# Performance work log

Measured on AMD Instinct MI355X. Metric: run time of the kernel, lower is better.

The kernel has to match this reference:

```python
import jax, jax.numpy as jnp
import numpy as np

N = 50000          # nodes
E = 1_600_000      # edges (avg degree 32)
IN = 16            # in_node_features
H0 = 64            # hidden_features_mlp[0]
D = 32             # hidden_features_mlp[1] == hidden_features_gnn
HF = 64            # hidden_final
OUT = 3            # out_features (congestion classes)
L = 3              # gnn_layer_num
EPS = 1e-5


def gelu(x):
    return jax.nn.gelu(x, approximate=False)  # torch nn.GELU default (erf)


def bn_eval(x, g, b):
    # BatchNorm1d in eval mode with fresh running stats (mean=0, var=1)
    return x * (g / jnp.sqrt(1.0 + EPS)) + b


def ln(x, g, b):
    m = jnp.mean(x, axis=-1, keepdims=True)
    v = jnp.var(x, axis=-1, keepdims=True)
    return (x - m) / jnp.sqrt(v + EPS) * g + b


def setup_inputs() -> dict:
    key = jax.random.key(0)
    ks = jax.random.split(key, 24)
    s = 0.1
    inp = {
        "x": jax.random.normal(ks[0], (N, IN), dtype=jnp.float32),
        "edge_index": jax.random.randint(ks[1], (2, E), 0, N, dtype=jnp.int32),
        # node_emb_mlp
        "emb_W1": jax.random.normal(ks[2], (IN, H0), dtype=jnp.float32) * s,
        "emb_b1": jnp.zeros((H0,), jnp.float32),
        "emb_bn1_g": jnp.ones((H0,), jnp.float32),
        "emb_bn1_b": jnp.zeros((H0,), jnp.float32),
        "emb_W2": jax.random.normal(ks[3], (H0, D), dtype=jnp.float32) * s,
        "emb_b2": jnp.zeros((D,), jnp.float32),
        "emb_bn2_g": jnp.ones((D,), jnp.float32),
        "emb_bn2_b": jnp.zeros((D,), jnp.float32),
        # GNN layers (stacked over L)
        "msg_W": jax.random.normal(ks[4], (L, 2 * D, D), dtype=jnp.float32) * s,
        "msg_b": jnp.zeros((L, D), jnp.float32),
        "msg_ln_g": jnp.ones((L, D), jnp.float32),
        "msg_ln_b": jnp.zeros((L, D), jnp.float32),
        "upd_W": jax.random.normal(ks[5], (L, 2 * D, D), dtype=jnp.float32) * s,
        "upd_b": jnp.zeros((L, D), jnp.float32),
        "upd_ln_g": jnp.ones((L, D), jnp.float32),
        "upd_ln_b": jnp.zeros((L, D), jnp.float32),
        # final_aggregation_layer
        "fin_W1": jax.random.normal(ks[6], (D, HF), dtype=jnp.float32) * s,
        "fin_b1": jnp.zeros((HF,), jnp.float32),
        "fin_bn_g": jnp.ones((HF,), jnp.float32),
        "fin_bn_b": jnp.zeros((HF,), jnp.float32),
        "fin_W2": jax.random.normal(ks[7], (HF, OUT), dtype=jnp.float32) * s,
        "fin_b2": jnp.zeros((OUT,), jnp.float32),
    }
    return inp


def reference(x, edge_index,
              emb_W1, emb_b1, emb_bn1_g, emb_bn1_b,
              emb_W2, emb_b2, emb_bn2_g, emb_bn2_b,
              msg_W, msg_b, msg_ln_g, msg_ln_b,
              upd_W, upd_b, upd_ln_g, upd_ln_b,
              fin_W1, fin_b1, fin_bn_g, fin_bn_b, fin_W2, fin_b2):
    src = edge_index[0]  # x_j (source, messages flow source->target)
    dst = edge_index[1]  # x_i (target, aggregation index)

    # node embedding MLP (dropout = identity in eval)
    h = gelu(bn_eval(x @ emb_W1 + emb_b1, emb_bn1_g, emb_bn1_b))
    h = gelu(bn_eval(h @ emb_W2 + emb_b2, emb_bn2_g, emb_bn2_b))
    pre = h

    for l in range(L):
        x_i = h[dst]  # [E, D]
        x_j = h[src]  # [E, D]
        m = gelu(ln(jnp.concatenate([x_i, x_j], axis=-1) @ msg_W[l] + msg_b[l],
                    msg_ln_g[l], msg_ln_b[l]))                 # [E, D]
        agg = jax.ops.segment_sum(m, dst, num_segments=N)      # [N, D]
        h = h + gelu(ln(jnp.concatenate([h, agg], axis=-1) @ upd_W[l] + upd_b[l],
                        upd_ln_g[l], upd_ln_b[l]))

    h = h + pre  # residual around the GNN stack

    general_emb = h[dst] - h[src]  # node_emb_j - node_emb_i, [E, D]
    out = gelu(bn_eval(general_emb @ fin_W1 + fin_b1, fin_bn_g, fin_bn_b))
    out = out @ fin_W2 + fin_b2  # [E, OUT] cc_scores
    return out
```

## Files before the change

### kernel.cpp

```cpp
#include <hip/hip_runtime.h>

#define NN 50000
#define NE 1600000
constexpr float LN_EPS = 1e-5f;

typedef _Float16 half8 __attribute__((ext_vector_type(8)));

__device__ __forceinline__ float gelu_f(float x){
  float ax = fabsf(x) * 0.70710678118654752440f;
  float t  = __builtin_amdgcn_rcpf(fmaf(0.3275911f, ax, 1.0f));
  float e  = __expf(-ax*ax);
  float p  = t*fmaf(t, fmaf(t, fmaf(t, fmaf(t, 1.061405429f, -1.453152027f),
                                    1.421413741f), -0.284496736f), 0.254829592f);
  float er = fmaf(-p, e, 1.0f);
  return 0.5f * x * (1.0f + copysignf(er, x));
}

__global__ __launch_bounds__(256) void hist_kernel(const int* __restrict__ ei,
    int* __restrict__ cnt, int* __restrict__ rank){
  int t = blockIdx.x*256 + threadIdx.x;
  if(t < NE/4){
    int4 d = ((const int4*)(ei + NE))[t];
    int4 r;
    r.x = atomicAdd(&cnt[d.x],1);
    r.y = atomicAdd(&cnt[d.y],1);
    r.z = atomicAdd(&cnt[d.z],1);
    r.w = atomicAdd(&cnt[d.w],1);
    ((int4*)rank)[t] = r;
  }
}

#define CHUNK 52
__global__ __launch_bounds__(1024) void scan_kernel(const int* __restrict__ deg, int* __restrict__ row_ptr){
  __shared__ int sums[1024];
  int t = threadIdx.x;
  int base = t*CHUNK;
  int4 v[13];
  int ssum = 0;
  #pragma unroll
  for(int i=0;i<13;i++){
    int idx = base + 4*i;
    if(idx + 3 < NN){
      v[i] = ((const int4*)deg)[(base>>2)+i];
    } else {
      v[i].x = (idx+0<NN)?deg[idx+0]:0; v[i].y = (idx+1<NN)?deg[idx+1]:0;
      v[i].z = (idx+2<NN)?deg[idx+2]:0; v[i].w = (idx+3<NN)?deg[idx+3]:0;
    }
    ssum += v[i].x + v[i].y + v[i].z + v[i].w;
  }
  sums[t]=ssum;
  __syncthreads();
  for(int off=1; off<1024; off<<=1){
    int vv = (t>=off) ? sums[t-off] : 0;
    __syncthreads();
    sums[t] += vv;
    __syncthreads();
  }
  int run = (t>0) ? sums[t-1] : 0;
  #pragma unroll
  for(int i=0;i<13;i++){
    int idx = base + 4*i;
    int4 o;
    o.x = run; run += v[i].x;
    o.y = run; run += v[i].y;
    o.z = run; run += v[i].z;
    o.w = run; run += v[i].w;
    if(idx + 3 < NN){
      ((int4*)row_ptr)[(base>>2)+i] = o;
    } else {
      if(idx+0<NN) row_ptr[idx+0]=o.x;
      if(idx+1<NN) row_ptr[idx+1]=o.y;
      if(idx+2<NN) row_ptr[idx+2]=o.z;
      if(idx+3<NN) row_ptr[idx+3]=o.w;
    }
  }
  if(t==1023) row_ptr[NN] = sums[1023];
}

__global__ __launch_bounds__(256) void fill_kernel(const int* __restrict__ ei,
    const int* __restrict__ row_ptr, const int* __restrict__ rank, int* __restrict__ csr_src){
  int t = blockIdx.x*256 + threadIdx.x;
  if(t < NE/4){
    int4 d  = ((const int4*)(ei + NE))[t];
    int4 sv = ((const int4*)ei)[t];
    int4 rk = ((const int4*)rank)[t];
    csr_src[row_ptr[d.x] + rk.x] = sv.x;
    csr_src[row_ptr[d.y] + rk.y] = sv.y;
    csr_src[row_ptr[d.z] + rk.z] = sv.z;
    csr_src[row_ptr[d.w] + rk.w] = sv.w;
  }
}

__global__ __launch_bounds__(256) void embed_pqr_kernel(
    const float* __restrict__ x,
    const float* __restrict__ W1, const float* __restrict__ b1,
    const float* __restrict__ g1, const float* __restrict__ bb1,
    const float* __restrict__ W2, const float* __restrict__ b2,
    const float* __restrict__ g2, const float* __restrict__ bb2,
    const float* __restrict__ Wm, const float* __restrict__ bm,
    const float* __restrict__ Wu, const float* __restrict__ bu,
    const float* __restrict__ fb1, const float* __restrict__ fbng, const float* __restrict__ fbnb,
    float* __restrict__ h, float* __restrict__ pre,
    float* __restrict__ P, _Float16* __restrict__ Qh, float* __restrict__ R,
    float* __restrict__ cvec)
{
  int n = blockIdx.x*256 + threadIdx.x;
  const float rs = rsqrtf(1.0f + LN_EPS);
  if(n < 64) cvec[n] = fmaf(fb1[n], fbng[n]*rs, fbnb[n]);
  if(n >= NN) return;
  float xv[16];
  const float4* xp = (const float4*)(x + (size_t)n*16);
  #pragma unroll
  for(int i=0;i<4;i++){ float4 t=xp[i]; xv[4*i]=t.x; xv[4*i+1]=t.y; xv[4*i+2]=t.z; xv[4*i+3]=t.w; }
  float a1[64];
  #pragma unroll
  for(int j=0;j<64;j++) a1[j]=b1[j];
  #pragma unroll
  for(int k=0;k<16;k++){
    float xk=xv[k];
    #pragma unroll
    for(int j=0;j<64;j++) a1[j] += xk * W1[k*64+j];
  }
  #pragma unroll
  for(int j=0;j<64;j++) a1[j] = gelu_f(a1[j]*(g1[j]*rs) + bb1[j]);
  float hv[32];
  #pragma unroll
  for(int j=0;j<32;j++) hv[j]=b2[j];
  #pragma unroll
  for(int k=0;k<64;k++){
    float tk=a1[k];
    #pragma unroll
    for(int j=0;j<32;j++) hv[j] += tk * W2[k*32+j];
  }
  #pragma unroll
  for(int j=0;j<32;j++){
    hv[j] = gelu_f(hv[j]*(g2[j]*rs) + bb2[j]);
    h[(size_t)n*32+j]=hv[j]; pre[(size_t)n*32+j]=hv[j];
  }
  float ap[32], aq[32], ar[32];
  #pragma unroll
  for(int j=0;j<32;j++){ ap[j]=bm[j]; aq[j]=0.f; ar[j]=bu[j]; }
  #pragma unroll
  for(int k=0;k<32;k++){
    float hk = hv[k];
    #pragma unroll
    for(int j=0;j<32;j++){
      ap[j] += hk * Wm[k*32+j];
      aq[j] += hk * Wm[(32+k)*32+j];
      ar[j] += hk * Wu[k*32+j];
    }
  }
  #pragma unroll
  for(int j=0;j<32;j++){ P[(size_t)n*32+j]=ap[j]; R[(size_t)n*32+j]=ar[j]; }
  half8* qo = (half8*)(Qh + (size_t)n*32);
  #pragma unroll
  for(int i=0;i<4;i++){
    half8 q;
    #pragma unroll
    for(int k=0;k<8;k++) q[k] = (_Float16)aq[8*i+k];
    qo[i] = q;
  }
}

__global__ __launch_bounds__(256) void msg_kernel(
    const float* __restrict__ P, const _Float16* __restrict__ Qh,
    const int* __restrict__ row_ptr, const int* __restrict__ csr_src,
    const float* __restrict__ mg, const float* __restrict__ mb,
    float* __restrict__ aggO)
{
  int tid = blockIdx.x*256 + threadIdx.x;
  int n = tid >> 4;
  int s = tid & 15;
  int slot = s >> 2;
  int q = s & 3;
  float4 mg0 = *(const float4*)(mg + q*8);
  float4 mg1 = *(const float4*)(mg + q*8 + 4);
  float4 mb0 = *(const float4*)(mb + q*8);
  float4 mb1 = *(const float4*)(mb + q*8 + 4);
  float mgq[8] = {mg0.x,mg0.y,mg0.z,mg0.w,mg1.x,mg1.y,mg1.z,mg1.w};
  float mbq[8] = {mb0.x,mb0.y,mb0.z,mb0.w,mb1.x,mb1.y,mb1.z,mb1.w};
  float4 pl0 = *(const float4*)(P + (size_t)n*32 + q*8);
  float4 pl1 = *(const float4*)(P + (size_t)n*32 + q*8 + 4);
  float p8[8] = {pl0.x,pl0.y,pl0.z,pl0.w,pl1.x,pl1.y,pl1.z,pl1.w};
  float agg8[8] = {0,0,0,0,0,0,0,0};
  int e0 = row_ptr[n], e1 = row_ptr[n+1];
  int e = e0 + slot;
  int src = (e < e1) ? csr_src[e] : 0;
  half8 qv = *(const half8*)(Qh + (size_t)src*32 + q*8);
  while(e < e1){
    int e2 = e + 4;
    int src2 = (e2 < e1) ? csr_src[e2] : 0;
    half8 qv2 = *(const half8*)(Qh + (size_t)src2*32 + q*8);
    float v[8];
    #pragma unroll
    for(int k=0;k<8;k++) v[k] = p8[k] + (float)qv[k];
    float ps = ((v[0]+v[1])+(v[2]+v[3])) + ((v[4]+v[5])+(v[6]+v[7]));
    ps += __shfl_xor(ps,1); ps += __shfl_xor(ps,2);
    float mean = ps * 0.03125f;
    float vs = 0.f;
    #pragma unroll
    for(int k=0;k<8;k++){ float dd = v[k]-mean; vs += dd*dd; v[k]=dd; }
    vs += __shfl_xor(vs,1); vs += __shfl_xor(vs,2);
    float rstd = rsqrtf(vs*0.03125f + LN_EPS);
    #pragma unroll
    for(int k=0;k<8;k++) agg8[k] += gelu_f(v[k]*rstd*mgq[k] + mbq[k]);
    qv = qv2; e = e2;
  }
  #pragma unroll
  for(int k=0;k<8;k++) agg8[k] += __shfl_xor(agg8[k], 4);
  #pragma unroll
  for(int k=0;k<8;k++) agg8[k] += __shfl_xor(agg8[k], 8);
  if(slot==0){
    float4 s0; s0.x=agg8[0]; s0.y=agg8[1]; s0.z=agg8[2]; s0.w=agg8[3];
    float4 s1; s1.x=agg8[4]; s1.y=agg8[5]; s1.z=agg8[6]; s1.w=agg8[7];
    *(float4*)(aggO + (size_t)n*32 + q*8)     = s0;
    *(float4*)(aggO + (size_t)n*32 + q*8 + 4) = s1;
  }
}

__global__ __launch_bounds__(256) void upd_pqr_kernel(
    const float* __restrict__ aggI, const float* __restrict__ Rio,
    const float* __restrict__ Ub,
    const float* __restrict__ ug, const float* __restrict__ ub,
    const float* __restrict__ Wm2, const float* __restrict__ bm2,
    const float* __restrict__ Wu2, const float* __restrict__ bu2,
    float* __restrict__ h,
    float* __restrict__ P, _Float16* __restrict__ Qh, float* __restrict__ Rout)
{
  int n = blockIdx.x*256 + threadIdx.x;
  if(n >= NN) return;
  float agg[32], u[32];
  const float4* ap4 = (const float4*)(aggI + (size_t)n*32);
  const float4* rp4 = (const float4*)(Rio + (size_t)n*32);
  #pragma unroll
  for(int i=0;i<8;i++){ float4 t=ap4[i]; agg[4*i]=t.x; agg[4*i+1]=t.y; agg[4*i+2]=t.z; agg[4*i+3]=t.w; }
  #pragma unroll
  for(int i=0;i<8;i++){ float4 t=rp4[i]; u[4*i]=t.x; u[4*i+1]=t.y; u[4*i+2]=t.z; u[4*i+3]=t.w; }
  #pragma unroll
  for(int k=0;k<32;k++){
    float a = agg[k];
    #pragma unroll
    for(int j=0;j<32;j++) u[j] += a * Ub[k*32+j];
  }
  float s0=0,s1=0,s2=0,s3=0;
  #pragma unroll
  for(int i=0;i<8;i++){ s0+=u[4*i]; s1+=u[4*i+1]; s2+=u[4*i+2]; s3+=u[4*i+3]; }
  float mean = ((s0+s1)+(s2+s3)) * 0.03125f;
  s0=s1=s2=s3=0.f;
  #pragma unroll
  for(int i=0;i<8;i++){
    float d0=u[4*i]-mean, d1=u[4*i+1]-mean, d2=u[4*i+2]-mean, d3=u[4*i+3]-mean;
    s0+=d0*d0; s1+=d1*d1; s2+=d2*d2; s3+=d3*d3;
    u[4*i]=d0; u[4*i+1]=d1; u[4*i+2]=d2; u[4*i+3]=d3;
  }
  float rstd = rsqrtf(((s0+s1)+(s2+s3))*0.03125f + LN_EPS);
  float hv[32];
  const float4* hp4 = (const float4*)(h + (size_t)n*32);
  #pragma unroll
  for(int i=0;i<8;i++){ float4 t=hp4[i]; hv[4*i]=t.x; hv[4*i+1]=t.y; hv[4*i+2]=t.z; hv[4*i+3]=t.w; }
  #pragma unroll
  for(int j=0;j<32;j++) hv[j] += gelu_f(u[j]*rstd*ug[j] + ub[j]);
  float4* ho = (float4*)(h + (size_t)n*32);
  #pragma unroll
  for(int i=0;i<8;i++){ float4 t; t.x=hv[4*i]; t.y=hv[4*i+1]; t.z=hv[4*i+2]; t.w=hv[4*i+3]; ho[i]=t; }
  float pq[32], qq[32], rr[32];
  #pragma unroll
  for(int j=0;j<32;j++){ pq[j]=bm2[j]; qq[j]=0.f; rr[j]=bu2[j]; }
  #pragma unroll
  for(int k=0;k<32;k++){
    float hk = hv[k];
    #pragma unroll
    for(int j=0;j<32;j++){
      pq[j] += hk * Wm2[k*32+j];
      qq[j] += hk * Wm2[(32+k)*32+j];
      rr[j] += hk * Wu2[k*32+j];
    }
  }
  #pragma unroll
  for(int j=0;j<32;j++){ P[(size_t)n*32+j]=pq[j]; Rout[(size_t)n*32+j]=rr[j]; }
  half8* qo = (half8*)(Qh + (size_t)n*32);
  #pragma unroll
  for(int i=0;i<4;i++){
    half8 q;
    #pragma unroll
    for(int k=0;k<8;k++) q[k] = (_Float16)qq[8*i+k];
    qo[i] = q;
  }
}

__global__ __launch_bounds__(256) void upd_fin_kernel(
    const float* __restrict__ aggI, const float* __restrict__ Rio,
    const float* __restrict__ Ub,
    const float* __restrict__ ug, const float* __restrict__ ub,
    const float* __restrict__ h, const float* __restrict__ pre,
    const float* __restrict__ fW1, const float* __restrict__ fbng,
    _Float16* __restrict__ y1, _Float16* __restrict__ y2)
{
  int n = blockIdx.x*256 + threadIdx.x;
  if(n >= NN) return;
  const float rs = rsqrtf(1.0f + LN_EPS);
  float agg[32], u[32];
  const float4* ap4 = (const float4*)(aggI + (size_t)n*32);
  const float4* rp4 = (const float4*)(Rio + (size_t)n*32);
  #pragma unroll
  for(int i=0;i<8;i++){ float4 t=ap4[i]; agg[4*i]=t.x; agg[4*i+1]=t.y; agg[4*i+2]=t.z; agg[4*i+3]=t.w; }
  #pragma unroll
  for(int i=0;i<8;i++){ float4 t=rp4[i]; u[4*i]=t.x; u[4*i+1]=t.y; u[4*i+2]=t.z; u[4*i+3]=t.w; }
  #pragma unroll
  for(int k=0;k<32;k++){
    float a = agg[k];
    #pragma unroll
    for(int j=0;j<32;j++) u[j] += a * Ub[k*32+j];
  }
  float s0=0,s1=0,s2=0,s3=0;
  #pragma unroll
  for(int i=0;i<8;i++){ s0+=u[4*i]; s1+=u[4*i+1]; s2+=u[4*i+2]; s3+=u[4*i+3]; }
  float mean = ((s0+s1)+(s2+s3)) * 0.03125f;
  s0=s1=s2=s3=0.f;
  #pragma unroll
  for(int i=0;i<8;i++){
    float d0=u[4*i]-mean, d1=u[4*i+1]-mean, d2=u[4*i+2]-mean, d3=u[4*i+3]-mean;
    s0+=d0*d0; s1+=d1*d1; s2+=d2*d2; s3+=d3*d3;
    u[4*i]=d0; u[4*i+1]=d1; u[4*i+2]=d2; u[4*i+3]=d3;
  }
  float rstd = rsqrtf(((s0+s1)+(s2+s3))*0.03125f + LN_EPS);
  float hv[32];
  const float4* hp4 = (const float4*)(h + (size_t)n*32);
  const float4* pp4 = (const float4*)(pre + (size_t)n*32);
  #pragma unroll
  for(int i=0;i<8;i++){ float4 t=hp4[i]; hv[4*i]=t.x; hv[4*i+1]=t.y; hv[4*i+2]=t.z; hv[4*i+3]=t.w; }
  #pragma unroll
  for(int j=0;j<32;j++) hv[j] += gelu_f(u[j]*rstd*ug[j] + ub[j]);
  #pragma unroll
  for(int i=0;i<8;i++){ float4 t=pp4[i]; hv[4*i]+=t.x; hv[4*i+1]+=t.y; hv[4*i+2]+=t.z; hv[4*i+3]+=t.w; }
  float acc[64];
  #pragma unroll
  for(int j=0;j<64;j++) acc[j]=0.f;
  #pragma unroll
  for(int k=0;k<32;k++){
    float hk = hv[k];
    #pragma unroll
    for(int j=0;j<64;j++) acc[j] += hk * fW1[k*64+j];
  }
  half8* yo1 = (half8*)(y1 + (size_t)n*32);
  half8* yo2 = (half8*)(y2 + (size_t)n*32);
  #pragma unroll
  for(int i=0;i<4;i++){
    half8 qa, qb;
    #pragma unroll
    for(int k=0;k<8;k++){
      qa[k] = (_Float16)(acc[8*i+k]    * (fbng[8*i+k]*rs));
      qb[k] = (_Float16)(acc[32+8*i+k] * (fbng[32+8*i+k]*rs));
    }
    yo1[i] = qa; yo2[i] = qb;
  }
}

__global__ __launch_bounds__(256) void finalA_kernel(
    const _Float16* __restrict__ y, const int* __restrict__ ei,
    const float* __restrict__ cvec, const float* __restrict__ W2,
    const float* __restrict__ b2, float* __restrict__ out)
{
  int t = blockIdx.x*256 + threadIdx.x;
  int e = t >> 2, q = t & 3;
  int s = __builtin_nontemporal_load(ei + e);
  int d = __builtin_nontemporal_load(ei + NE + e);
  half8 a8 = *(const half8*)(y + (size_t)d*32 + q*8);
  half8 c8 = *(const half8*)(y + (size_t)s*32 + q*8);
  float4 cv0 = *(const float4*)(cvec + q*8);
  float4 cv1 = *(const float4*)(cvec + q*8 + 4);
  float cq[8] = {cv0.x,cv0.y,cv0.z,cv0.w,cv1.x,cv1.y,cv1.z,cv1.w};
  const float4* wp = (const float4*)(W2 + q*24);
  float4 w0=wp[0], w1=wp[1], w2=wp[2], w3=wp[3], w4=wp[4], w5=wp[5];
  float w[24] = {w0.x,w0.y,w0.z,w0.w, w1.x,w1.y,w1.z,w1.w, w2.x,w2.y,w2.z,w2.w,
                 w3.x,w3.y,w3.z,w3.w, w4.x,w4.y,w4.z,w4.w, w5.x,w5.y,w5.z,w5.w};
  float o0=0.f,o1=0.f,o2=0.f;
  #pragma unroll
  for(int k=0;k<8;k++){
    float tt = gelu_f(((float)a8[k]-(float)c8[k]) + cq[k]);
    o0 += tt*w[3*k]; o1 += tt*w[3*k+1]; o2 += tt*w[3*k+2];
  }
  o0 += __shfl_xor(o0,1); o0 += __shfl_xor(o0,2);
  o1 += __shfl_xor(o1,1); o1 += __shfl_xor(o1,2);
  o2 += __shfl_xor(o2,1); o2 += __shfl_xor(o2,2);
  float ov = (q==0) ? o0 + b2[0] : (q==1) ? o1 + b2[1] : o2 + b2[2];
  if(q < 3) __builtin_nontemporal_store(ov, out + (size_t)e*3 + q);
}

__global__ __launch_bounds__(256) void finalB_kernel(
    const _Float16* __restrict__ y, const int* __restrict__ ei,
    const float* __restrict__ cvec,
    const float* __restrict__ W2,
    float* __restrict__ out)
{
  int t = blockIdx.x*256 + threadIdx.x;
  int e = t >> 2, q = t & 3;
  float prev = 0.f;
  if(q < 3) prev = __builtin_nontemporal_load(out + (size_t)e*3 + q);
  int s = __builtin_nontemporal_load(ei + e);
  int d = __builtin_nontemporal_load(ei + NE + e);
  half8 a8 = *(const half8*)(y + (size_t)d*32 + q*8);
  half8 c8 = *(const half8*)(y + (size_t)s*32 + q*8);
  float4 cv0 = *(const float4*)(cvec + q*8);
  float4 cv1 = *(const float4*)(cvec + q*8 + 4);
  float cq[8] = {cv0.x,cv0.y,cv0.z,cv0.w,cv1.x,cv1.y,cv1.z,cv1.w};
  const float4* wp = (const float4*)(W2 + q*24);
  float4 w0=wp[0], w1=wp[1], w2=wp[2], w3=wp[3], w4=wp[4], w5=wp[5];
  float w[24] = {w0.x,w0.y,w0.z,w0.w, w1.x,w1.y,w1.z,w1.w, w2.x,w2.y,w2.z,w2.w,
                 w3.x,w3.y,w3.z,w3.w, w4.x,w4.y,w4.z,w4.w, w5.x,w5.y,w5.z,w5.w};
  float o0=0.f,o1=0.f,o2=0.f;
  #pragma unroll
  for(int k=0;k<8;k++){
    float tt = gelu_f(((float)a8[k]-(float)c8[k]) + cq[k]);
    o0 += tt*w[3*k]; o1 += tt*w[3*k+1]; o2 += tt*w[3*k+2];
  }
  o0 += __shfl_xor(o0,1); o0 += __shfl_xor(o0,2);
  o1 += __shfl_xor(o1,1); o1 += __shfl_xor(o1,2);
  o2 += __shfl_xor(o2,1); o2 += __shfl_xor(o2,2);
  float ov = prev + ((q==0) ? o0 : (q==1) ? o1 : o2);
  if(q < 3) __builtin_nontemporal_store(ov, out + (size_t)e*3 + q);
}

extern "C" void kernel_launch(void* const* d_in, const int* in_sizes, int n_in,
                              void* d_out, int out_size, void* d_ws, size_t ws_size,
                              hipStream_t stream)
{
  (void)in_sizes; (void)n_in; (void)out_size; (void)ws_size;
  const float* x     = (const float*)d_in[0];
  const int*   ei    = (const int*)d_in[1];
  const float* eW1   = (const float*)d_in[2];
  const float* eb1   = (const float*)d_in[3];
  const float* ebn1g = (const float*)d_in[4];
  const float* ebn1b = (const float*)d_in[5];
  const float* eW2   = (const float*)d_in[6];
  const float* eb2   = (const float*)d_in[7];
  const float* ebn2g = (const float*)d_in[8];
  const float* ebn2b = (const float*)d_in[9];
  const float* msgW  = (const float*)d_in[10];
  const float* msgb  = (const float*)d_in[11];
  const float* msglng= (const float*)d_in[12];
  const float* msglnb= (const float*)d_in[13];
  const float* updW  = (const float*)d_in[14];
  const float* updb  = (const float*)d_in[15];
  const float* updlng= (const float*)d_in[16];
  const float* updlnb= (const float*)d_in[17];
  const float* fW1   = (const float*)d_in[18];
  const float* fb1   = (const float*)d_in[19];
  const float* fbng  = (const float*)d_in[20];
  const float* fbnb  = (const float*)d_in[21];
  const float* fW2   = (const float*)d_in[22];
  const float* fb2   = (const float*)d_in[23];
  float* out = (float*)d_out;

  float* f   = (float*)d_ws;
  float* h   = f;
  float* pre = f + 1*(size_t)NN*32;
  float* P   = f + 2*(size_t)NN*32;
  float* R   = f + 3*(size_t)NN*32;
  float* agg = f + 4*(size_t)NN*32;
  _Float16* Qh = (_Float16*)(f + 5*(size_t)NN*32);
  _Float16* y1 = (_Float16*)P;
  _Float16* y2 = y1 + (size_t)NN*32;
  int* ip      = (int*)(f + 5*(size_t)NN*32 + (size_t)NN*16);
  int* cnt     = ip;
  int* row_ptr = ip + NN;
  int* csr     = ip + 2*NN + 4;
  int* rank    = (int*)agg;
  float* cvec  = (float*)cnt;

  hipMemsetAsync(cnt, 0, NN*sizeof(int), stream);
  hist_kernel<<<(NE/4+255)/256, 256, 0, stream>>>(ei, cnt, rank);
  scan_kernel<<<1, 1024, 0, stream>>>(cnt, row_ptr);
  fill_kernel<<<(NE/4+255)/256, 256, 0, stream>>>(ei, row_ptr, rank, csr);

  embed_pqr_kernel<<<(NN+255)/256, 256, 0, stream>>>(x, eW1, eb1, ebn1g, ebn1b,
      eW2, eb2, ebn2g, ebn2b,
      msgW, msgb, updW, updb,
      fb1, fbng, fbnb,
      h, pre, P, Qh, R, cvec);

  for(int l=0; l<3; l++){
    msg_kernel<<<(NN*16)/256, 256, 0, stream>>>(P, Qh, row_ptr, csr,
        msglng + l*32, msglnb + l*32, agg);
    if(l < 2){
      upd_pqr_kernel<<<(NN+255)/256, 256, 0, stream>>>(agg, R,
          updW + l*2048 + 1024, updlng + l*32, updlnb + l*32,
          msgW + (l+1)*2048, msgb + (l+1)*32,
          updW + (l+1)*2048, updb + (l+1)*32,
          h, P, Qh, R);
    } else {
      upd_fin_kernel<<<(NN+255)/256, 256, 0, stream>>>(agg, R,
          updW + l*2048 + 1024, updlng + l*32, updlnb + l*32,
          h, pre, fW1, fbng, y1, y2);
    }
  }

  finalA_kernel<<<(NE*4)/256, 256, 0, stream>>>(y1, ei, cvec,      fW2,      fb2, out);
  finalB_kernel<<<(NE*4)/256, 256, 0, stream>>>(y2, ei, cvec + 32, fW2 + 96, out);
}
```

Before: 544.8 us.

## Split node MLPs across 4 lanes per node and fuse histogram with embedding

The per-node embedding, update and final-projection kernels now assign four lanes to each node, with lane shuffles broadcasting inputs, instead of one thread computing all 32–64 outputs. This cuts register pressure and raises occupancy and memory coalescing. The histogram pass and the embedding pass now run in a single launch by splitting the block range, which removes one launch and lets the two overlap. In exchange there is extra shuffle traffic, each lane re-reads the weight slices, and cvec moves to its own workspace slot so it no longer overlaps cnt.

```diff
diff --git a/kernel.cpp b/kernel.cpp
--- a/kernel.cpp
+++ b/kernel.cpp
@@ -2,6 +2,8 @@
 
 #define NN 50000
 #define NE 1600000
+#define HIST_B 1563
+#define EMB_B  782
 constexpr float LN_EPS = 1e-5f;
 
 typedef _Float16 half8 __attribute__((ext_vector_type(8)));
@@ -16,18 +18,109 @@
   return 0.5f * x * (1.0f + copysignf(er, x));
 }
 
-__global__ __launch_bounds__(256) void hist_kernel(const int* __restrict__ ei,
-    int* __restrict__ cnt, int* __restrict__ rank){
-  int t = blockIdx.x*256 + threadIdx.x;
-  if(t < NE/4){
-    int4 d = ((const int4*)(ei + NE))[t];
-    int4 r;
-    r.x = atomicAdd(&cnt[d.x],1);
-    r.y = atomicAdd(&cnt[d.y],1);
-    r.z = atomicAdd(&cnt[d.z],1);
-    r.w = atomicAdd(&cnt[d.w],1);
-    ((int4*)rank)[t] = r;
-  }
+__device__ __forceinline__ void ld8(const float* __restrict__ p, float* r){
+  float4 a=((const float4*)p)[0], b=((const float4*)p)[1];
+  r[0]=a.x;r[1]=a.y;r[2]=a.z;r[3]=a.w;r[4]=b.x;r[5]=b.y;r[6]=b.z;r[7]=b.w;
+}
+__device__ __forceinline__ void ld16(const float* __restrict__ p, float* r){ ld8(p,r); ld8(p+8,r+8); }
+__device__ __forceinline__ void st8(float* __restrict__ p, const float* r){
+  float4 a,b; a.x=r[0];a.y=r[1];a.z=r[2];a.w=r[3]; b.x=r[4];b.y=r[5];b.z=r[6];b.w=r[7];
+  ((float4*)p)[0]=a; ((float4*)p)[1]=b;
+}
+
+__global__ __launch_bounds__(256) void hist_embed_kernel(
+    const int* __restrict__ ei, int* __restrict__ cnt, int* __restrict__ rank,
+    const float* __restrict__ x,
+    const float* __restrict__ W1, const float* __restrict__ b1,
+    const float* __restrict__ g1, const float* __restrict__ bb1,
+    const float* __restrict__ W2, const float* __restrict__ b2,
+    const float* __restrict__ g2, const float* __restrict__ bb2,
+    const float* __restrict__ Wm, const float* __restrict__ bm,
+    const float* __restrict__ Wu, const float* __restrict__ bu,
+    const float* __restrict__ fb1, const float* __restrict__ fbng, const float* __restrict__ fbnb,
+    float* __restrict__ h, float* __restrict__ pre,
+    float* __restrict__ P, _Float16* __restrict__ Qh, float* __restrict__ R,
+    float* __restrict__ cvec)
+{
+  if(blockIdx.x < HIST_B){
+    int t = blockIdx.x*256 + threadIdx.x;
+    if(t < NE/4){
+      int4 d = ((const int4*)(ei + NE))[t];
+      int4 r;
+      r.x = atomicAdd(&cnt[d.x],1);
+      r.y = atomicAdd(&cnt[d.y],1);
+      r.z = atomicAdd(&cnt[d.z],1);
+      r.w = atomicAdd(&cnt[d.w],1);
+      ((int4*)rank)[t] = r;
+    }
+    return;
+  }
+  int t = (blockIdx.x - HIST_B)*256 + threadIdx.x;
+  const float rs = rsqrtf(1.0f + LN_EPS);
+  if(t < 64) cvec[t] = fmaf(fb1[t], fbng[t]*rs, fbnb[t]);
+  int n = t >> 2, q = t & 3;
+  if(n >= NN) return;
+  int base = threadIdx.x & 60;
+  float4 xq = ((const float4*)x)[n*4 + q];
+  float xv[16];
+  #pragma unroll
+  for(int m=0;m<4;m++){
+    xv[4*m+0]=__shfl(xq.x, base|m);
+    xv[4*m+1]=__shfl(xq.y, base|m);
+    xv[4*m+2]=__shfl(xq.z, base|m);
+    xv[4*m+3]=__shfl(xq.w, base|m);
+  }
+  float a1q[16]; ld16(b1 + q*16, a1q);
+  #pragma unroll
+  for(int k=0;k<16;k++){
+    float w[16]; ld16(W1 + k*64 + q*16, w);
+    float xk = xv[k];
+    #pragma unroll
+    for(int j=0;j<16;j++) a1q[j] += xk * w[j];
+  }
+  { float g[16], b[16]; ld16(g1+q*16,g); ld16(bb1+q*16,b);
+    #pragma unroll
+    for(int j=0;j<16;j++) a1q[j] = gelu_f(a1q[j]*(g[j]*rs) + b[j]); }
+  float hq[8]; ld8(b2 + q*8, hq);
+  #pragma unroll
+  for(int m=0;m<4;m++){
+    #pragma unroll
+    for(int kk=0;kk<16;kk++){
+      float a = __shfl(a1q[kk], base|m);
+      float w[8]; ld8(W2 + (m*16+kk)*32 + q*8, w);
+      #pragma unroll
+      for(int j=0;j<8;j++) hq[j] += a * w[j];
+    }
+  }
+  { float g[8], b[8]; ld8(g2+q*8,g); ld8(bb2+q*8,b);
+    #pragma unroll
+    for(int j=0;j<8;j++) hq[j] = gelu_f(hq[j]*(g[j]*rs) + b[j]); }
+  st8(h   + (size_t)n*32 + q*8, hq);
+  st8(pre + (size_t)n*32 + q*8, hq);
+  float apv[8], aqv[8], arv[8];
+  ld8(bm+q*8, apv); ld8(bu+q*8, arv);
+  #pragma unroll
+  for(int j=0;j<8;j++) aqv[j]=0.f;
+  #pragma unroll
+  for(int m=0;m<4;m++){
+    #pragma unroll
+    for(int kk=0;kk<8;kk++){
+      float hk = __shfl(hq[kk], base|m);
+      int k = m*8+kk;
+      float wm[8],wq[8],wu[8];
+      ld8(Wm + k*32      + q*8, wm);
+      ld8(Wm + (32+k)*32 + q*8, wq);
+      ld8(Wu + k*32      + q*8, wu);
+      #pragma unroll
+      for(int j=0;j<8;j++){ apv[j]+=hk*wm[j]; aqv[j]+=hk*wq[j]; arv[j]+=hk*wu[j]; }
+    }
+  }
+  st8(P + (size_t)n*32 + q*8, apv);
+  st8(R + (size_t)n*32 + q*8, arv);
+  half8 qo;
+  #pragma unroll
+  for(int k=0;k<8;k++) qo[k] = (_Float16)aqv[k];
+  *(half8*)(Qh + (size_t)n*32 + q*8) = qo;
 }
 
 #define CHUNK 52
@@ -91,77 +184,6 @@
   }
 }
 
-__global__ __launch_bounds__(256) void embed_pqr_kernel(
-    const float* __restrict__ x,
-    const float* __restrict__ W1, const float* __restrict__ b1,
-    const float* __restrict__ g1, const float* __restrict__ bb1,
-    const float* __restrict__ W2, const float* __restrict__ b2,
-    const float* __restrict__ g2, const float* __restrict__ bb2,
-    const float* __restrict__ Wm, const float* __restrict__ bm,
-    const float* __restrict__ Wu, const float* __restrict__ bu,
-    const float* __restrict__ fb1, const float* __restrict__ fbng, const float* __restrict__ fbnb,
-    float* __restrict__ h, float* __restrict__ pre,
-    float* __restrict__ P, _Float16* __restrict__ Qh, float* __restrict__ R,
-    float* __restrict__ cvec)
-{
-  int n = blockIdx.x*256 + threadIdx.x;
-  const float rs = rsqrtf(1.0f + LN_EPS);
-  if(n < 64) cvec[n] = fmaf(fb1[n], fbng[n]*rs, fbnb[n]);
-  if(n >= NN) return;
-  float xv[16];
-  const float4* xp = (const float4*)(x + (size_t)n*16);
-  #pragma unroll
-  for(int i=0;i<4;i++){ float4 t=xp[i]; xv[4*i]=t.x; xv[4*i+1]=t.y; xv[4*i+2]=t.z; xv[4*i+3]=t.w; }
-  float a1[64];
-  #pragma unroll
-  for(int j=0;j<64;j++) a1[j]=b1[j];
-  #pragma unroll
-  for(int k=0;k<16;k++){
-    float xk=xv[k];
-    #pragma unroll
-    for(int j=0;j<64;j++) a1[j] += xk * W1[k*64+j];
-  }
-  #pragma unroll
-  for(int j=0;j<64;j++) a1[j] = gelu_f(a1[j]*(g1[j]*rs) + bb1[j]);
-  float hv[32];
-  #pragma unroll
-  for(int j=0;j<32;j++) hv[j]=b2[j];
-  #pragma unroll
-  for(int k=0;k<64;k++){
-    float tk=a1[k];
-    #pragma unroll
-    for(int j=0;j<32;j++) hv[j] += tk * W2[k*32+j];
-  }
-  #pragma unroll
-  for(int j=0;j<32;j++){
-    hv[j] = gelu_f(hv[j]*(g2[j]*rs) + bb2[j]);
-    h[(size_t)n*32+j]=hv[j]; pre[(size_t)n*32+j]=hv[j];
-  }
-  float ap[32], aq[32], ar[32];
-  #pragma unroll
-  for(int j=0;j<32;j++){ ap[j]=bm[j]; aq[j]=0.f; ar[j]=bu[j]; }
-  #pragma unroll
-  for(int k=0;k<32;k++){
-    float hk = hv[k];
-    #pragma unroll
-    for(int j=0;j<32;j++){
-      ap[j] += hk * Wm[k*32+j];
-      aq[j] += hk * Wm[(32+k)*32+j];
-      ar[j] += hk * Wu[k*32+j];
-    }
-  }
-  #pragma unroll
-  for(int j=0;j<32;j++){ P[(size_t)n*32+j]=ap[j]; R[(size_t)n*32+j]=ar[j]; }
-  half8* qo = (half8*)(Qh + (size_t)n*32);
-  #pragma unroll
-  for(int i=0;i<4;i++){
-    half8 q;
-    #pragma unroll
-    for(int k=0;k<8;k++) q[k] = (_Float16)aq[8*i+k];
-    qo[i] = q;
-  }
-}
-
 __global__ __launch_bounds__(256) void msg_kernel(
     const float* __restrict__ P, const _Float16* __restrict__ Qh,
     const int* __restrict__ row_ptr, const int* __restrict__ csr_src,
@@ -173,15 +195,9 @@
   int s = tid & 15;
   int slot = s >> 2;
   int q = s & 3;
-  float4 mg0 = *(const float4*)(mg + q*8);
-  float4 mg1 = *(const float4*)(mg + q*8 + 4);
-  float4 mb0 = *(const float4*)(mb + q*8);
-  float4 mb1 = *(const float4*)(mb + q*8 + 4);
-  float mgq[8] = {mg0.x,mg0.y,mg0.z,mg0.w,mg1.x,mg1.y,mg1.z,mg1.w};
-  float mbq[8] = {mb0.x,mb0.y,mb0.z,mb0.w,mb1.x,mb1.y,mb1.z,mb1.w};
-  float4 pl0 = *(const float4*)(P + (size_t)n*32 + q*8);
-  float4 pl1 = *(const float4*)(P + (size_t)n*32 + q*8 + 4);
-  float p8[8] = {pl0.x,pl0.y,pl0.z,pl0.w,pl1.x,pl1.y,pl1.z,pl1.w};
+  float mgq[8], mbq[8], p8[8];
+  ld8(mg + q*8, mgq); ld8(mb + q*8, mbq);
+  ld8(P + (size_t)n*32 + q*8, p8);
   float agg8[8] = {0,0,0,0,0,0,0,0};
   int e0 = row_ptr[n], e1 = row_ptr[n+1];
   int e = e0 + slot;
@@ -210,12 +226,7 @@
   for(int k=0;k<8;k++) agg8[k] += __shfl_xor(agg8[k], 4);
   #pragma unroll
   for(int k=0;k<8;k++) agg8[k] += __shfl_xor(agg8[k], 8);
-  if(slot==0){
-    float4 s0; s0.x=agg8[0]; s0.y=agg8[1]; s0.z=agg8[2]; s0.w=agg8[3];
-    float4 s1; s1.x=agg8[4]; s1.y=agg8[5]; s1.z=agg8[6]; s1.w=agg8[7];
-    *(float4*)(aggO + (size_t)n*32 + q*8)     = s0;
-    *(float4*)(aggO + (size_t)n*32 + q*8 + 4) = s1;
-  }
+  if(slot==0) st8(aggO + (size_t)n*32 + q*8, agg8);
 }
 
 __global__ __launch_bounds__(256) void upd_pqr_kernel(
@@ -227,65 +238,61 @@
     float* __restrict__ h,
     float* __restrict__ P, _Float16* __restrict__ Qh, float* __restrict__ Rout)
 {
-  int n = blockIdx.x*256 + threadIdx.x;
+  int t = blockIdx.x*256 + threadIdx.x;
+  int n = t >> 2, q = t & 3;
   if(n >= NN) return;
-  float agg[32], u[32];
-  const float4* ap4 = (const float4*)(aggI + (size_t)n*32);
-  const float4* rp4 = (const float4*)(Rio + (size_t)n*32);
-  #pragma unroll
-  for(int i=0;i<8;i++){ float4 t=ap4[i]; agg[4*i]=t.x; agg[4*i+1]=t.y; agg[4*i+2]=t.z; agg[4*i+3]=t.w; }
-  #pragma unroll
-  for(int i=0;i<8;i++){ float4 t=rp4[i]; u[4*i]=t.x; u[4*i+1]=t.y; u[4*i+2]=t.z; u[4*i+3]=t.w; }
-  #pragma unroll
-  for(int k=0;k<32;k++){
-    float a = agg[k];
-    #pragma unroll
-    for(int j=0;j<32;j++) u[j] += a * Ub[k*32+j];
-  }
-  float s0=0,s1=0,s2=0,s3=0;
-  #pragma unroll
-  for(int i=0;i<8;i++){ s0+=u[4*i]; s1+=u[4*i+1]; s2+=u[4*i+2]; s3+=u[4*i+3]; }
-  float mean = ((s0+s1)+(s2+s3)) * 0.03125f;
-  s0=s1=s2=s3=0.f;
-  #pragma unroll
-  for(int i=0;i<8;i++){
-    float d0=u[4*i]-mean, d1=u[4*i+1]-mean, d2=u[4*i+2]-mean, d3=u[4*i+3]-mean;
-    s0+=d0*d0; s1+=d1*d1; s2+=d2*d2; s3+=d3*d3;
-    u[4*i]=d0; u[4*i+1]=d1; u[4*i+2]=d2; u[4*i+3]=d3;
-  }
-  float rstd = rsqrtf(((s0+s1)+(s2+s3))*0.03125f + LN_EPS);
-  float hv[32];
-  const float4* hp4 = (const float4*)(h + (size_t)n*32);
-  #pragma unroll
-  for(int i=0;i<8;i++){ float4 t=hp4[i]; hv[4*i]=t.x; hv[4*i+1]=t.y; hv[4*i+2]=t.z; hv[4*i+3]=t.w; }
-  #pragma unroll
-  for(int j=0;j<32;j++) hv[j] += gelu_f(u[j]*rstd*ug[j] + ub[j]);
-  float4* ho = (float4*)(h + (size_t)n*32);
-  #pragma unroll
-  for(int i=0;i<8;i++){ float4 t; t.x=hv[4*i]; t.y=hv[4*i+1]; t.z=hv[4*i+2]; t.w=hv[4*i+3]; ho[i]=t; }
-  float pq[32], qq[32], rr[32];
-  #pragma unroll
-  for(int j=0;j<32;j++){ pq[j]=bm2[j]; qq[j]=0.f; rr[j]=bu2[j]; }
-  #pragma unroll
-  for(int k=0;k<32;k++){
-    float hk = hv[k];
-    #pragma unroll
-    for(int j=0;j<32;j++){
-      pq[j] += hk * Wm2[k*32+j];
-      qq[j] += hk * Wm2[(32+k)*32+j];
-      rr[j] += hk * Wu2[k*32+j];
-    }
-  }
-  #pragma unroll
-  for(int j=0;j<32;j++){ P[(size_t)n*32+j]=pq[j]; Rout[(size_t)n*32+j]=rr[j]; }
-  half8* qo = (half8*)(Qh + (size_t)n*32);
-  #pragma unroll
-  for(int i=0;i<4;i++){
-    half8 q;
-    #pragma unroll
-    for(int k=0;k<8;k++) q[k] = (_Float16)qq[8*i+k];
-    qo[i] = q;
-  }
+  int base = threadIdx.x & 60;
+  float aggq[8], uq[8];
+  ld8(aggI + (size_t)n*32 + q*8, aggq);
+  ld8(Rio  + (size_t)n*32 + q*8, uq);
+  #pragma unroll
+  for(int m=0;m<4;m++){
+    #pragma unroll
+    for(int kk=0;kk<8;kk++){
+      float a = __shfl(aggq[kk], base|m);
+      float w[8]; ld8(Ub + (m*8+kk)*32 + q*8, w);
+      #pragma unroll
+      for(int j=0;j<8;j++) uq[j] += a * w[j];
+    }
+  }
+  float sm = ((uq[0]+uq[1])+(uq[2]+uq[3])) + ((uq[4]+uq[5])+(uq[6]+uq[7]));
+  sm += __shfl_xor(sm,1); sm += __shfl_xor(sm,2);
+  float mean = sm * 0.03125f;
+  float vs = 0.f;
+  #pragma unroll
+  for(int j=0;j<8;j++){ float d = uq[j]-mean; vs += d*d; uq[j]=d; }
+  vs += __shfl_xor(vs,1); vs += __shfl_xor(vs,2);
+  float rstd = rsqrtf(vs*0.03125f + LN_EPS);
+  float ugq[8], ubq[8], hq[8];
+  ld8(ug+q*8, ugq); ld8(ub+q*8, ubq);
+  ld8(h + (size_t)n*32 + q*8, hq);
+  #pragma unroll
+  for(int j=0;j<8;j++) hq[j] += gelu_f(uq[j]*rstd*ugq[j] + ubq[j]);
+  st8(h + (size_t)n*32 + q*8, hq);
+  float apv[8], aqv[8], arv[8];
+  ld8(bm2+q*8, apv); ld8(bu2+q*8, arv);
+  #pragma unroll
+  for(int j=0;j<8;j++) aqv[j]=0.f;
+  #pragma unroll
+  for(int m=0;m<4;m++){
+    #pragma unroll
+    for(int kk=0;kk<8;kk++){
+      float hk = __shfl(hq[kk], base|m);
+      int k = m*8+kk;
+      float wm[8],wq[8],wu[8];
+      ld8(Wm2 + k*32      + q*8, wm);
+      ld8(Wm2 + (32+k)*32 + q*8, wq);
+      ld8(Wu2 + k*32      + q*8, wu);
+      #pragma unroll
+      for(int j=0;j<8;j++){ apv[j]+=hk*wm[j]; aqv[j]+=hk*wq[j]; arv[j]+=hk*wu[j]; }
+    }
+  }
+  st8(P    + (size_t)n*32 + q*8, apv);
+  st8(Rout + (size_t)n*32 + q*8, arv);
+  half8 qo;
+  #pragma unroll
+  for(int k=0;k<8;k++) qo[k] = (_Float16)aqv[k];
+  *(half8*)(Qh + (size_t)n*32 + q*8) = qo;
 }
 
 __global__ __launch_bounds__(256) void upd_fin_kernel(
@@ -296,64 +303,60 @@
     const float* __restrict__ fW1, const float* __restrict__ fbng,
     _Float16* __restrict__ y1, _Float16* __restrict__ y2)
 {
-  int n = blockIdx.x*256 + threadIdx.x;
+  int t = blockIdx.x*256 + threadIdx.x;
+  int n = t >> 2, q = t & 3;
   if(n >= NN) return;
+  int base = threadIdx.x & 60;
   const float rs = rsqrtf(1.0f + LN_EPS);
-  float agg[32], u[32];
-  const float4* ap4 = (const float4*)(aggI + (size_t)n*32);
-  const float4* rp4 = (const float4*)(Rio + (size_t)n*32);
-  #pragma unroll
-  for(int i=0;i<8;i++){ float4 t=ap4[i]; agg[4*i]=t.x; agg[4*i+1]=t.y; agg[4*i+2]=t.z; agg[4*i+3]=t.w; }
-  #pragma unroll
-  for(int i=0;i<8;i++){ float4 t=rp4[i]; u[4*i]=t.x; u[4*i+1]=t.y; u[4*i+2]=t.z; u[4*i+3]=t.w; }
-  #pragma unroll
-  for(int k=0;k<32;k++){
-    float a = agg[k];
-    #pragma unroll
-    for(int j=0;j<32;j++) u[j] += a * Ub[k*32+j];
-  }
-  float s0=0,s1=0,s2=0,s3=0;
-  #pragma unroll
-  for(int i=0;i<8;i++){ s0+=u[4*i]; s1+=u[4*i+1]; s2+=u[4*i+2]; s3+=u[4*i+3]; }
-  float mean = ((s0+s1)+(s2+s3)) * 0.03125f;
-  s0=s1=s2=s3=0.f;
-  #pragma unroll
-  for(int i=0;i<8;i++){
-    float d0=u[4*i]-mean, d1=u[4*i+1]-mean, d2=u[4*i+2]-mean, d3=u[4*i+3]-mean;
-    s0+=d0*d0; s1+=d1*d1; s2+=d2*d2; s3+=d3*d3;
-    u[4*i]=d0; u[4*i+1]=d1; u[4*i+2]=d2; u[4*i+3]=d3;
-  }
-  float rstd = rsqrtf(((s0+s1)+(s2+s3))*0.03125f + LN_EPS);
-  float hv[32];
-  const float4* hp4 = (const float4*)(h + (size_t)n*32);
-  const float4* pp4 = (const float4*)(pre + (size_t)n*32);
-  #pragma unroll
-  for(int i=0;i<8;i++){ float4 t=hp4[i]; hv[4*i]=t.x; hv[4*i+1]=t.y; hv[4*i+2]=t.z; hv[4*i+3]=t.w; }
-  #pragma unroll
-  for(int j=0;j<32;j++) hv[j] += gelu_f(u[j]*rstd*ug[j] + ub[j]);
-  #pragma unroll
-  for(int i=0;i<8;i++){ float4 t=pp4[i]; hv[4*i]+=t.x; hv[4*i+1]+=t.y; hv[4*i+2]+=t.z; hv[4*i+3]+=t.w; }
-  float acc[64];
-  #pragma unroll
-  for(int j=0;j<64;j++) acc[j]=0.f;
-  #pragma unroll
-  for(int k=0;k<32;k++){
-    float hk = hv[k];
-    #pragma unroll
-    for(int j=0;j<64;j++) acc[j] += hk * fW1[k*64+j];
-  }
-  half8* yo1 = (half8*)(y1 + (size_t)n*32);
-  half8* yo2 = (half8*)(y2 + (size_t)n*32);
-  #pragma unroll
-  for(int i=0;i<4;i++){
-    half8 qa, qb;
-    #pragma unroll
-    for(int k=0;k<8;k++){
-      qa[k] = (_Float16)(acc[8*i+k]    * (fbng[8*i+k]*rs));
-      qb[k] = (_Float16)(acc[32+8*i+k] * (fbng[32+8*i+k]*rs));
-    }
-    yo1[i] = qa; yo2[i] = qb;
-  }
+  float aggq[8], uq[8];
+  ld8(aggI + (size_t)n*32 + q*8, aggq);
+  ld8(Rio  + (size_t)n*32 + q*8, uq);
+  #pragma unroll
+  for(int m=0;m<4;m++){
+    #pragma unroll
+    for(int kk=0;kk<8;kk++){
+      float a = __shfl(aggq[kk], base|m);
+      float w[8]; ld8(Ub + (m*8+kk)*32 + q*8, w);
+      #pragma unroll
+      for(int j=0;j<8;j++) uq[j] += a * w[j];
+    }
+  }
+  float sm = ((uq[0]+uq[1])+(uq[2]+uq[3])) + ((uq[4]+uq[5])+(uq[6]+uq[7]));
+  sm += __shfl_xor(sm,1); sm += __shfl_xor(sm,2);
+  float mean = sm * 0.03125f;
+  float vs = 0.f;
+  #pragma unroll
+  for(int j=0;j<8;j++){ float d = uq[j]-mean; vs += d*d; uq[j]=d; }
+  vs += __shfl_xor(vs,1); vs += __shfl_xor(vs,2);
+  float rstd = rsqrtf(vs*0.03125f + LN_EPS);
+  float ugq[8], ubq[8], hq[8], pq[8];
+  ld8(ug+q*8, ugq); ld8(ub+q*8, ubq);
+  ld8(h   + (size_t)n*32 + q*8, hq);
+  ld8(pre + (size_t)n*32 + q*8, pq);
+  #pragma unroll
+  for(int j=0;j<8;j++) hq[j] += gelu_f(uq[j]*rstd*ugq[j] + ubq[j]) + pq[j];
+  float acc[16];
+  #pragma unroll
+  for(int j=0;j<16;j++) acc[j]=0.f;
+  #pragma unroll
+  for(int m=0;m<4;m++){
+    #pragma unroll
+    for(int kk=0;kk<8;kk++){
+      float hk = __shfl(hq[kk], base|m);
+      float w[16]; ld16(fW1 + (m*8+kk)*64 + q*16, w);
+      #pragma unroll
+      for(int j=0;j<16;j++) acc[j] += hk * w[j];
+    }
+  }
+  float fg[16]; ld16(fbng + q*16, fg);
+  half8 o0, o1;
+  #pragma unroll
+  for(int k=0;k<8;k++){
+    o0[k] = (_Float16)(acc[k]   * (fg[k]*rs));
+    o1[k] = (_Float16)(acc[8+k] * (fg[8+k]*rs));
+  }
+  _Float16* dst = (q<2) ? (y1 + (size_t)n*32 + q*16) : (y2 + (size_t)n*32 + (q-2)*16);
+  ((half8*)dst)[0] = o0; ((half8*)dst)[1] = o1;
 }
 
 __global__ __launch_bounds__(256) void finalA_kernel(
@@ -367,13 +370,8 @@
   int d = __builtin_nontemporal_load(ei + NE + e);
   half8 a8 = *(const half8*)(y + (size_t)d*32 + q*8);
   half8 c8 = *(const half8*)(y + (size_t)s*32 + q*8);
-  float4 cv0 = *(const float4*)(cvec + q*8);
-  float4 cv1 = *(const float4*)(cvec + q*8 + 4);
-  float cq[8] = {cv0.x,cv0.y,cv0.z,cv0.w,cv1.x,cv1.y,cv1.z,cv1.w};
-  const float4* wp = (const float4*)(W2 + q*24);
-  float4 w0=wp[0], w1=wp[1], w2=wp[2], w3=wp[3], w4=wp[4], w5=wp[5];
-  float w[24] = {w0.x,w0.y,w0.z,w0.w, w1.x,w1.y,w1.z,w1.w, w2.x,w2.y,w2.z,w2.w,
-                 w3.x,w3.y,w3.z,w3.w, w4.x,w4.y,w4.z,w4.w, w5.x,w5.y,w5.z,w5.w};
+  float cq[8]; ld8(cvec + q*8, cq);
+  float w[24]; ld8(W2+q*24, w); ld8(W2+q*24+8, w+8); ld8(W2+q*24+16, w+16);
   float o0=0.f,o1=0.f,o2=0.f;
   #pragma unroll
   for(int k=0;k<8;k++){
@@ -389,8 +387,7 @@
 
 __global__ __launch_bounds__(256) void finalB_kernel(
     const _Float16* __restrict__ y, const int* __restrict__ ei,
-    const float* __restrict__ cvec,
-    const float* __restrict__ W2,
+    const float* __restrict__ cvec, const float* __restrict__ W2,
     float* __restrict__ out)
 {
   int t = blockIdx.x*256 + threadIdx.x;
@@ -401,13 +398,8 @@
   int d = __builtin_nontemporal_load(ei + NE + e);
   half8 a8 = *(const half8*)(y + (size_t)d*32 + q*8);
   half8 c8 = *(const half8*)(y + (size_t)s*32 + q*8);
-  float4 cv0 = *(const float4*)(cvec + q*8);
-  float4 cv1 = *(const float4*)(cvec + q*8 + 4);
-  float cq[8] = {cv0.x,cv0.y,cv0.z,cv0.w,cv1.x,cv1.y,cv1.z,cv1.w};
-  const float4* wp = (const float4*)(W2 + q*24);
-  float4 w0=wp[0], w1=wp[1], w2=wp[2], w3=wp[3], w4=wp[4], w5=wp[5];
-  float w[24] = {w0.x,w0.y,w0.z,w0.w, w1.x,w1.y,w1.z,w1.w, w2.x,w2.y,w2.z,w2.w,
-                 w3.x,w3.y,w3.z,w3.w, w4.x,w4.y,w4.z,w4.w, w5.x,w5.y,w5.z,w5.w};
+  float cq[8]; ld8(cvec + q*8, cq);
+  float w[24]; ld8(W2+q*24, w); ld8(W2+q*24+8, w+8); ld8(W2+q*24+16, w+16);
   float o0=0.f,o1=0.f,o2=0.f;
   #pragma unroll
   for(int k=0;k<8;k++){
@@ -461,35 +453,33 @@
   _Float16* Qh = (_Float16*)(f + 5*(size_t)NN*32);
   _Float16* y1 = (_Float16*)P;
   _Float16* y2 = y1 + (size_t)NN*32;
-  int* ip      = (int*)(f + 5*(size_t)NN*32 + (size_t)NN*16);
+  float* cvec  = f + 5*(size_t)NN*32 + (size_t)NN*16;
+  int* ip      = (int*)(cvec + 64);
   int* cnt     = ip;
   int* row_ptr = ip + NN;
   int* csr     = ip + 2*NN + 4;
   int* rank    = (int*)agg;
-  float* cvec  = (float*)cnt;
 
   hipMemsetAsync(cnt, 0, NN*sizeof(int), stream);
-  hist_kernel<<<(NE/4+255)/256, 256, 0, stream>>>(ei, cnt, rank);
-  scan_kernel<<<1, 1024, 0, stream>>>(cnt, row_ptr);
-  fill_kernel<<<(NE/4+255)/256, 256, 0, stream>>>(ei, row_ptr, rank, csr);
-
-  embed_pqr_kernel<<<(NN+255)/256, 256, 0, stream>>>(x, eW1, eb1, ebn1g, ebn1b,
-      eW2, eb2, ebn2g, ebn2b,
+  hist_embed_kernel<<<HIST_B + EMB_B, 256, 0, stream>>>(ei, cnt, rank,
+      x, eW1, eb1, ebn1g, ebn1b, eW2, eb2, ebn2g, ebn2b,
       msgW, msgb, updW, updb,
       fb1, fbng, fbnb,
       h, pre, P, Qh, R, cvec);
+  scan_kernel<<<1, 1024, 0, stream>>>(cnt, row_ptr);
+  fill_kernel<<<HIST_B, 256, 0, stream>>>(ei, row_ptr, rank, csr);
 
   for(int l=0; l<3; l++){
     msg_kernel<<<(NN*16)/256, 256, 0, stream>>>(P, Qh, row_ptr, csr,
         msglng + l*32, msglnb + l*32, agg);
     if(l < 2){
-      upd_pqr_kernel<<<(NN+255)/256, 256, 0, stream>>>(agg, R,
+      upd_pqr_kernel<<<EMB_B, 256, 0, stream>>>(agg, R,
           updW + l*2048 + 1024, updlng + l*32, updlnb + l*32,
           msgW + (l+1)*2048, msgb + (l+1)*32,
           updW + (l+1)*2048, updb + (l+1)*32,
           h, P, Qh, R);
     } else {
-      upd_fin_kernel<<<(NN+255)/256, 256, 0, stream>>>(agg, R,
+      upd_fin_kernel<<<EMB_B, 256, 0, stream>>>(agg, R,
           updW + l*2048 + 1024, updlng + l*32, updlnb + l*32,
           h, pre, fW1, fbng, y1, y2);
     }
```

Result: faster. 517.1 us (-5.1%).
